# Optimization experiments

Measured on AMD Instinct MI355X. Metric: run time of the kernel, lower is better.

The kernel has to match this reference:

```python
import jax, jax.numpy as jnp
import numpy as np

D_MODEL = 1024
N_HEADS = 16
N_KV = 4
HEAD_DIM = D_MODEL // N_HEADS  # 64
EPS = 1e-5
THETA = 10000.0


def _rope_tables(S):
    half = HEAD_DIM // 2
    inv_freq = 1.0 / (THETA ** (jnp.arange(half, dtype=jnp.float32) / half))
    t = jnp.arange(S, dtype=jnp.float32)
    f = t[:, None] * inv_freq[None, :]  # [S, half]
    return jnp.cos(f), jnp.sin(f)


def _apply_rope(x, cos, sin):
    # x: [B, H, S, D]
    half = x.shape[-1] // 2
    x1, x2 = x[..., :half], x[..., half:]
    c = cos[None, None, :, :]
    s = sin[None, None, :, :]
    return jnp.concatenate([x1 * c - x2 * s, x1 * s + x2 * c], axis=-1)


def _rmsnorm(x, scale):
    rms = jnp.sqrt(jnp.mean(x * x, axis=-1, keepdims=True) + EPS)
    return x / rms * scale


def setup_inputs() -> dict:
    key = jax.random.key(0)
    ks = jax.random.split(key, 4)
    B, S = 2, 2048
    x = jax.random.normal(ks[0], (B, S, D_MODEL), dtype=jnp.float32)
    Wq = jax.random.normal(ks[1], (D_MODEL, D_MODEL), dtype=jnp.float32) * 0.02
    Wkv = jax.random.normal(ks[2], (D_MODEL, 2 * N_KV * HEAD_DIM), dtype=jnp.float32) * 0.02
    Wo = jax.random.normal(ks[3], (D_MODEL, D_MODEL), dtype=jnp.float32) * 0.02
    q_scale = jnp.ones((HEAD_DIM,), dtype=jnp.float32)
    k_scale = jnp.ones((HEAD_DIM,), dtype=jnp.float32)
    return {"x": x, "Wq": Wq, "Wkv": Wkv, "Wo": Wo,
            "q_scale": q_scale, "k_scale": k_scale}


def reference(x, Wq, Wkv, Wo, q_scale, k_scale):
    B, S, D = x.shape
    groups = N_HEADS // N_KV  # GQA group size

    # projections
    q = (x @ Wq).reshape(B, S, N_HEADS, HEAD_DIM).transpose(0, 2, 1, 3)  # [B,H,S,d]
    kv = x @ Wkv
    k, v = jnp.split(kv, 2, axis=-1)
    k = k.reshape(B, S, N_KV, HEAD_DIM).transpose(0, 2, 1, 3)  # [B,Hkv,S,d]
    v = v.reshape(B, S, N_KV, HEAD_DIM).transpose(0, 2, 1, 3)

    # per-head QK-RMSNorm (before RoPE, as in the torch module)
    q = _rmsnorm(q, q_scale)
    k = _rmsnorm(k, k_scale)

    # RoPE
    cos, sin = _rope_tables(S)
    q = _apply_rope(q, cos, sin)
    k = _apply_rope(k, cos, sin)

    # causal GQA attention (equivalent to SDPA with enable_gqa=True)
    qg = q.reshape(B, N_KV, groups, S, HEAD_DIM)
    scale = 1.0 / np.sqrt(HEAD_DIM).astype(np.float32)
    scores = jnp.einsum('bkgsd,bktd->bkgst', qg, k) * scale  # [B,Hkv,g,S,S]
    causal = jnp.tril(jnp.ones((S, S), dtype=bool))
    scores = jnp.where(causal[None, None, None], scores, -jnp.inf)
    attn = jax.nn.softmax(scores, axis=-1)
    out = jnp.einsum('bkgst,bktd->bkgsd', attn, v)
    out = out.reshape(B, N_HEADS, S, HEAD_DIM).transpose(0, 2, 1, 3).reshape(B, S, D)
    return out @ Wo
```

## Files before the change

kernel.cpp:

```cpp
#include <hip/hip_runtime.h>

#define S_LEN 2048
#define BATCH 2
#define DM    1024
#define NH    16
#define NKV   4
#define HD    64
#define MROWS (BATCH * S_LEN)
#define NQKV  1536

typedef __attribute__((ext_vector_type(8))) short bf16x8;
typedef __attribute__((ext_vector_type(4))) short s16x4;
typedef __attribute__((ext_vector_type(4))) float f32x4;

__device__ __forceinline__ unsigned short f2bf(float f) {
  unsigned int u = __float_as_uint(f);
  u += 0x7FFF + ((u >> 16) & 1);
  return (unsigned short)(u >> 16);
}

__device__ __forceinline__ void gload_lds16(const unsigned short* g, unsigned short* l) {
  __builtin_amdgcn_global_load_lds((const __attribute__((address_space(1))) void*)g,
                                   (__attribute__((address_space(3))) void*)l, 16, 0, 0);
}
__device__ __forceinline__ void gload_lds4(const unsigned short* g, unsigned short* l) {
  __builtin_amdgcn_global_load_lds((const __attribute__((address_space(1))) void*)g,
                                   (__attribute__((address_space(3))) void*)l, 4, 0, 0);
}

__global__ __launch_bounds__(256) void cvt_x_kernel(const float* __restrict__ x,
                                                    unsigned short* __restrict__ xb, int n) {
  int i = (blockIdx.x * 256 + threadIdx.x) * 4;
  if (i < n) {
    float4 v = *reinterpret_cast<const float4*>(x + i);
    xb[i + 0] = f2bf(v.x);
    xb[i + 1] = f2bf(v.y);
    xb[i + 2] = f2bf(v.z);
    xb[i + 3] = f2bf(v.w);
  }
}

__global__ __launch_bounds__(256) void transpose_all_kernel(const float* __restrict__ Wq,
                                                            const float* __restrict__ Wkv,
                                                            const float* __restrict__ Wo,
                                                            unsigned short* __restrict__ wt1,
                                                            unsigned short* __restrict__ wot) {
  __shared__ float tile[64][65];
  int bid = blockIdx.x;
  const float* in;
  unsigned short* out;
  int R, C, bx, by;
  if (bid < 256) { in = Wq; out = wt1; R = 1024; C = 1024; bx = bid & 15; by = bid >> 4; }
  else if (bid < 384) { int k = bid - 256; in = Wkv; out = wt1 + 1024 * 1024; R = 1024; C = 512; bx = k & 7; by = k >> 3; }
  else { int k = bid - 384; in = Wo; out = wot; R = 1024; C = 1024; bx = k & 15; by = k >> 4; }
  int r0 = by * 64, c0 = bx * 64;
  int t = threadIdx.x;
  int rl = t >> 2, cs = (t & 3) * 16;
#pragma unroll
  for (int k = 0; k < 4; ++k) {
    float4 v = *reinterpret_cast<const float4*>(in + (size_t)(r0 + rl) * C + c0 + cs + 4 * k);
    tile[rl][cs + 4 * k + 0] = v.x;
    tile[rl][cs + 4 * k + 1] = v.y;
    tile[rl][cs + 4 * k + 2] = v.z;
    tile[rl][cs + 4 * k + 3] = v.w;
  }
  __syncthreads();
  int cl = t >> 2, rs = (t & 3) * 16;
  bf16x8 v0, v1;
#pragma unroll
  for (int i = 0; i < 8; ++i) v0[i] = (short)f2bf(tile[rs + i][cl]);
#pragma unroll
  for (int i = 0; i < 8; ++i) v1[i] = (short)f2bf(tile[rs + 8 + i][cl]);
  unsigned short* dst = out + (size_t)(c0 + cl) * R + r0 + rs;
  *reinterpret_cast<bf16x8*>(dst) = v0;
  *reinterpret_cast<bf16x8*>(dst + 8) = v1;
}

__global__ __launch_bounds__(256) void gemm1_fused(const unsigned short* __restrict__ A,
                                                   const unsigned short* __restrict__ BT,
                                                   const float* __restrict__ q_scale,
                                                   const float* __restrict__ k_scale,
                                                   unsigned short* __restrict__ qb,
                                                   unsigned short* __restrict__ kbuf,
                                                   unsigned short* __restrict__ vrow,
                                                   int K) {
  __shared__ __align__(16) unsigned short As[128 * 64];
  __shared__ __align__(16) unsigned short Bs[64 * 64];
  int bx = blockIdx.x;
  int row0 = blockIdx.y * 128, col0 = bx * 64;
  int t = threadIdx.x;
  int w = t >> 6, lane = t & 63, quad = lane >> 4, l16 = lane & 15;
  int srow = lane >> 3;
  int scol = (lane & 7) * 8;

  f32x4 acc[2][4];
#pragma unroll
  for (int i = 0; i < 2; ++i)
#pragma unroll
    for (int j = 0; j < 4; ++j) acc[i][j] = (f32x4){0.f, 0.f, 0.f, 0.f};

  for (int k0 = 0; k0 < K; k0 += 64) {
#pragma unroll
    for (int j = 0; j < 4; ++j)
      gload_lds16(A + (size_t)(row0 + w * 32 + j * 8 + srow) * K + k0 + scol,
                  &As[(w * 32 + j * 8) * 64]);
#pragma unroll
    for (int j = 0; j < 2; ++j)
      gload_lds16(BT + (size_t)(col0 + w * 16 + j * 8 + srow) * K + k0 + scol,
                  &Bs[(w * 16 + j * 8) * 64]);
    __syncthreads();
#pragma unroll
    for (int ks = 0; ks < 2; ++ks) {
      bf16x8 af[2], bfr[4];
#pragma unroll
      for (int i = 0; i < 2; ++i)
        af[i] = *reinterpret_cast<const bf16x8*>(&As[(w * 32 + i * 16 + l16) * 64 + ks * 32 + quad * 8]);
#pragma unroll
      for (int j = 0; j < 4; ++j)
        bfr[j] = *reinterpret_cast<const bf16x8*>(&Bs[(j * 16 + l16) * 64 + ks * 32 + quad * 8]);
#pragma unroll
      for (int i = 0; i < 2; ++i)
#pragma unroll
        for (int j = 0; j < 4; ++j)
          acc[i][j] = __builtin_amdgcn_mfma_f32_16x16x32_bf16(af[i], bfr[j], acc[i][j], 0, 0, 0);
    }
    __syncthreads();
  }

  if (bx < 20) {
    const float* scale = (bx < 16) ? q_scale : k_scale;
    float post = (bx < 16) ? 1.0f : 0.125f * 1.44269504088896f;
    float sc0 = scale[l16], sc1 = scale[16 + l16], sc2 = scale[32 + l16], sc3 = scale[48 + l16];
    float invf0 = exp2f((float)l16 * (-13.2877123795495f / 32.0f));
    float invf1 = exp2f((float)(l16 + 16) * (-13.2877123795495f / 32.0f));
#pragma unroll
    for (int i = 0; i < 2; ++i)
#pragma unroll
      for (int rg = 0; rg < 4; ++rg) {
        int row = row0 + w * 32 + i * 16 + quad * 4 + rg;
        int b = row >> 11, s = row & 2047;
        float v0 = acc[i][0][rg], v1 = acc[i][1][rg], v2 = acc[i][2][rg], v3 = acc[i][3][rg];
        float ss = v0 * v0 + v1 * v1 + v2 * v2 + v3 * v3;
        ss += __shfl_xor(ss, 1, 64);
        ss += __shfl_xor(ss, 2, 64);
        ss += __shfl_xor(ss, 4, 64);
        ss += __shfl_xor(ss, 8, 64);
        float inv_rms = 1.0f / sqrtf(ss * (1.0f / 64.0f) + 1e-5f);
        float n0 = v0 * inv_rms * sc0, n1 = v1 * inv_rms * sc1;
        float n2 = v2 * inv_rms * sc2, n3 = v3 * inv_rms * sc3;
        float f0 = (float)s * invf0, f1 = (float)s * invf1;
        float c0 = cosf(f0), s0 = sinf(f0), c1 = cosf(f1), s1 = sinf(f1);
        float o0 = (n0 * c0 - n2 * s0) * post;
        float o1 = (n1 * c1 - n3 * s1) * post;
        float o2 = (n0 * s0 + n2 * c0) * post;
        float o3 = (n1 * s1 + n3 * c1) * post;
        unsigned short* dst = (bx < 16)
            ? qb + ((size_t)(b * NH + bx) * S_LEN + s) * HD
            : kbuf + ((size_t)(b * NKV + (bx - 16)) * S_LEN + s) * HD;
        dst[l16] = f2bf(o0);
        dst[16 + l16] = f2bf(o1);
        dst[32 + l16] = f2bf(o2);
        dst[48 + l16] = f2bf(o3);
      }
  } else {
    int kvh = bx - 20;
#pragma unroll
    for (int i = 0; i < 2; ++i)
#pragma unroll
      for (int rg = 0; rg < 4; ++rg) {
        int row = row0 + w * 32 + i * 16 + quad * 4 + rg;
        unsigned short* dst = vrow + (size_t)row * 256 + kvh * 64;
        dst[l16] = f2bf(acc[i][0][rg]);
        dst[16 + l16] = f2bf(acc[i][1][rg]);
        dst[32 + l16] = f2bf(acc[i][2][rg]);
        dst[48 + l16] = f2bf(acc[i][3][rg]);
      }
  }
}

__global__ __launch_bounds__(256) void v_transpose_bf16(const unsigned short* __restrict__ vrow,
                                                        unsigned short* __restrict__ vt) {
  __shared__ unsigned short tile[64][72];
  int bkv = blockIdx.x >> 5;
  int b = bkv >> 2, kvh = bkv & 3;
  int s0 = (blockIdx.x & 31) * 64;
  int t = threadIdx.x;
  int sl = t >> 2, part = (t & 3) * 16;
  const unsigned short* src = vrow + (size_t)(b * S_LEN + s0 + sl) * 256 + kvh * 64 + part;
  *reinterpret_cast<bf16x8*>(&tile[sl][part]) = *reinterpret_cast<const bf16x8*>(src);
  *reinterpret_cast<bf16x8*>(&tile[sl][part + 8]) = *reinterpret_cast<const bf16x8*>(src + 8);
  __syncthreads();
  int d = t >> 2, sc = (t & 3) * 16;
  bf16x8 a0, a1;
#pragma unroll
  for (int i = 0; i < 8; ++i) a0[i] = (short)tile[sc + i][d];
#pragma unroll
  for (int i = 0; i < 8; ++i) a1[i] = (short)tile[sc + 8 + i][d];
  unsigned short* dst = vt + ((size_t)bkv * 64 + d) * S_LEN + s0 + sc;
  *reinterpret_cast<bf16x8*>(dst) = a0;
  *reinterpret_cast<bf16x8*>(dst + 8) = a1;
}

#define CH 136
#define TILE_SH (32 * CH)
__global__ __launch_bounds__(256, 3) void attn_kernel(const unsigned short* __restrict__ qb,
                                                      const unsigned short* __restrict__ kbuf,
                                                      const unsigned short* __restrict__ vt,
                                                      unsigned short* __restrict__ Opart,
                                                      float* __restrict__ lpart) {
  __shared__ __align__(16) unsigned short Ks[2][TILE_SH];
  __shared__ __align__(16) unsigned short Vs[2][TILE_SH];
  __shared__ __align__(16) unsigned short PT[4][2][16][72];
  const size_t OZ = (size_t)BATCH * NH * S_LEN * HD;
  const size_t LZ = (size_t)BATCH * NH * S_LEN;
  int t32 = 63 - (int)(blockIdx.x >> 4);
  int sub = blockIdx.x & 15;
  int z = sub & 1;
  int bkv = sub >> 1;
  int b = bkv >> 2, kvh = bkv & 3;
  int w = threadIdx.x >> 6;
  int h = kvh * 4 + w;
  int lane = threadIdx.x & 63;
  int quad = lane >> 4, l16 = lane & 15;
  int qa = t32 * 32 + l16;
  const unsigned short* Q = qb + (size_t)(b * NH + h) * S_LEN * HD;
  const unsigned short* Kh = kbuf + (size_t)(b * NKV + kvh) * S_LEN * HD;
  const unsigned short* Vh = vt + (size_t)(b * NKV + kvh) * HD * S_LEN;

  bf16x8 bqa0 = *reinterpret_cast<const bf16x8*>(Q + (size_t)qa * HD + quad * 8);
  bf16x8 bqa1 = *reinterpret_cast<const bf16x8*>(Q + (size_t)qa * HD + 32 + quad * 8);
  bf16x8 bqb0 = *reinterpret_cast<const bf16x8*>(Q + (size_t)(qa + 16) * HD + quad * 8);
  bf16x8 bqb1 = *reinterpret_cast<const bf16x8*>(Q + (size_t)(qa + 16) * HD + 32 + quad * 8);

  bf16x8 ones;
#pragma unroll
  for (int i = 0; i < 8; ++i) ones[i] = (short)0x3F80;

  f32x4 ot[2][4];
#pragma unroll
  for (int gq = 0; gq < 2; ++gq)
#pragma unroll
    for (int i = 0; i < 4; ++i) ot[gq][i] = (f32x4){0.f, 0.f, 0.f, 0.f};
  f32x4 ol[2] = {(f32x4){0.f, 0.f, 0.f, 0.f}, (f32x4){0.f, 0.f, 0.f, 0.f}};

  int n = (t32 >> 1) + 1;

  auto stage = [&](int kbase, int dbuf) {
    const unsigned short* kg = Kh + (size_t)(kbase + w * 16) * HD + lane * 2;
    const unsigned short* vg = Vh + (size_t)(w * 16 + (lane >> 5)) * S_LEN + kbase + (lane & 31) * 2;
    unsigned short* kl = &Ks[dbuf][(w * 8) * CH];
    unsigned short* vl = &Vs[dbuf][(w * 8) * CH];
#pragma unroll
    for (int c = 0; c < 8; ++c) {
      gload_lds4(kg + (size_t)(2 * c) * HD, kl + c * CH);
      gload_lds4(vg + (size_t)(2 * c) * S_LEN, vl + c * CH);
    }
  };

  if (z < n) {
    stage(z << 6, 0);
    __syncthreads();

    for (int kb = z; kb < n; kb += 2) {
      int dbuf = (kb >> 1) & 1;
      bool diag = (kb == n - 1);
      if (kb + 2 < n) stage((kb + 2) << 6, dbuf ^ 1);
      int kbase = kb << 6;
      const unsigned short* Kd = Ks[dbuf];
      const unsigned short* Vd = Vs[dbuf];

      f32x4 sa[4], sb[4];
#pragma unroll
      for (int km = 0; km < 4; ++km) {
        int ch = km * 8 + (l16 >> 1);
        int base = ch * CH + (l16 & 1) * 64;
        bf16x8 k0 = *reinterpret_cast<const bf16x8*>(&Kd[base + quad * 8]);
        bf16x8 k1 = *reinterpret_cast<const bf16x8*>(&Kd[base + 32 + quad * 8]);
        f32x4 s = {0.f, 0.f, 0.f, 0.f};
        s = __builtin_amdgcn_mfma_f32_16x16x32_bf16(k0, bqa0, s, 0, 0, 0);
        s = __builtin_amdgcn_mfma_f32_16x16x32_bf16(k1, bqa1, s, 0, 0, 0);
        sa[km] = s;
        f32x4 s2 = {0.f, 0.f, 0.f, 0.f};
        s2 = __builtin_amdgcn_mfma_f32_16x16x32_bf16(k0, bqb0, s2, 0, 0, 0);
        s2 = __builtin_amdgcn_mfma_f32_16x16x32_bf16(k1, bqb1, s2, 0, 0, 0);
        sb[km] = s2;
      }
      if (diag) {
#pragma unroll
        for (int km = 0; km < 4; ++km)
#pragma unroll
          for (int rg = 0; rg < 4; ++rg) {
            int key = kbase + km * 16 + quad * 4 + rg;
            if (key > qa) sa[km][rg] = -1e30f;
            if (key > qa + 16) sb[km][rg] = -1e30f;
          }
      }
#pragma unroll
      for (int km = 0; km < 4; ++km) {
        float a0 = exp2f(sa[km][0]), a1 = exp2f(sa[km][1]);
        float a2 = exp2f(sa[km][2]), a3 = exp2f(sa[km][3]);
        uint2 pw;
        pw.x = __builtin_amdgcn_perm(__float_as_uint(a1), __float_as_uint(a0), 0x07060302);
        pw.y = __builtin_amdgcn_perm(__float_as_uint(a3), __float_as_uint(a2), 0x07060302);
        *reinterpret_cast<uint2*>(&PT[w][0][l16][km * 16 + quad * 4]) = pw;
        float b0 = exp2f(sb[km][0]), b1 = exp2f(sb[km][1]);
        float b2 = exp2f(sb[km][2]), b3 = exp2f(sb[km][3]);
        uint2 qw;
        qw.x = __builtin_amdgcn_perm(__float_as_uint(b1), __float_as_uint(b0), 0x07060302);
        qw.y = __builtin_amdgcn_perm(__float_as_uint(b3), __float_as_uint(b2), 0x07060302);
        *reinterpret_cast<uint2*>(&PT[w][1][l16][km * 16 + quad * 4]) = qw;
      }
      bf16x8 pa0 = *reinterpret_cast<const bf16x8*>(&PT[w][0][l16][quad * 8]);
      bf16x8 pa1 = *reinterpret_cast<const bf16x8*>(&PT[w][0][l16][32 + quad * 8]);
      bf16x8 pb0 = *reinterpret_cast<const bf16x8*>(&PT[w][1][l16][quad * 8]);
      bf16x8 pb1 = *reinterpret_cast<const bf16x8*>(&PT[w][1][l16][32 + quad * 8]);
      ol[0] = __builtin_amdgcn_mfma_f32_16x16x32_bf16(ones, pa0, ol[0], 0, 0, 0);
      ol[0] = __builtin_amdgcn_mfma_f32_16x16x32_bf16(ones, pa1, ol[0], 0, 0, 0);
      ol[1] = __builtin_amdgcn_mfma_f32_16x16x32_bf16(ones, pb0, ol[1], 0, 0, 0);
      ol[1] = __builtin_amdgcn_mfma_f32_16x16x32_bf16(ones, pb1, ol[1], 0, 0, 0);
#pragma unroll
      for (int dm = 0; dm < 4; ++dm) {
        int ch = dm * 8 + (l16 >> 1);
        int base = ch * CH + (l16 & 1) * 64;
        bf16x8 v0 = *reinterpret_cast<const bf16x8*>(&Vd[base + quad * 8]);
        bf16x8 v1 = *reinterpret_cast<const bf16x8*>(&Vd[base + 32 + quad * 8]);
        ot[0][dm] = __builtin_amdgcn_mfma_f32_16x16x32_bf16(v0, pa0, ot[0][dm], 0, 0, 0);
        ot[0][dm] = __builtin_amdgcn_mfma_f32_16x16x32_bf16(v1, pa1, ot[0][dm], 0, 0, 0);
        ot[1][dm] = __builtin_amdgcn_mfma_f32_16x16x32_bf16(v0, pb0, ot[1][dm], 0, 0, 0);
        ot[1][dm] = __builtin_amdgcn_mfma_f32_16x16x32_bf16(v1, pb1, ot[1][dm], 0, 0, 0);
      }
      __syncthreads();
    }
  }

  unsigned short* Oz = Opart + (size_t)z * OZ;
  float* lz = lpart + (size_t)z * LZ;
#pragma unroll
  for (int gq = 0; gq < 2; ++gq) {
    size_t base = ((size_t)(b * NH + h) * S_LEN + qa + gq * 16) * HD;
#pragma unroll
    for (int dm = 0; dm < 4; ++dm) {
      s16x4 pv;
#pragma unroll
      for (int rg = 0; rg < 4; ++rg) pv[rg] = (short)f2bf(ot[gq][dm][rg]);
      *reinterpret_cast<s16x4*>(Oz + base + dm * 16 + quad * 4) = pv;
    }
  }
  if (quad == 0) {
    size_t lb = (size_t)(b * NH + h) * S_LEN + t32 * 32 + l16;
    lz[lb] = ol[0][0];
    lz[lb + 16] = ol[1][0];
  }
}

__global__ __launch_bounds__(256) void attn_combine_kernel(const unsigned short* __restrict__ Opart,
                                                           const float* __restrict__ lpart,
                                                           unsigned short* __restrict__ ctx) {
  const size_t OZ = (size_t)BATCH * NH * S_LEN * HD;
  const size_t LZ = (size_t)BATCH * NH * S_LEN;
  int i8 = blockIdx.x * 256 + threadIdx.x;
  size_t i = (size_t)i8 * 8;
  int row = i8 >> 3;
  bf16x8 a = *reinterpret_cast<const bf16x8*>(Opart + i);
  bf16x8 c = *reinterpret_cast<const bf16x8*>(Opart + OZ + i);
  float inv = 1.0f / (lpart[row] + lpart[LZ + row]);
  int q = row & 2047;
  int bh = row >> 11;
  int b = bh >> 4, h = bh & 15;
  int d0 = (i8 & 7) * 8;
  bf16x8 o;
#pragma unroll
  for (int k = 0; k < 8; ++k) {
    float fa = __uint_as_float(((unsigned int)(unsigned short)a[k]) << 16);
    float fc = __uint_as_float(((unsigned int)(unsigned short)c[k]) << 16);
    o[k] = (short)f2bf((fa + fc) * inv);
  }
  *reinterpret_cast<bf16x8*>(ctx + ((size_t)(b * S_LEN + q)) * DM + h * HD + d0) = o;
}

__global__ __launch_bounds__(256) void gemm_bt_n64(const unsigned short* __restrict__ A,
                                                   const unsigned short* __restrict__ BT,
                                                   float* __restrict__ C,
                                                   int M, int N, int K) {
  __shared__ __align__(16) unsigned short As[128 * 64];
  __shared__ __align__(16) unsigned short Bs[64 * 64];
  int row0 = blockIdx.y * 128, col0 = blockIdx.x * 64;
  int t = threadIdx.x;
  int w = t >> 6, lane = t & 63, quad = lane >> 4, l16 = lane & 15;
  int srow = lane >> 3;
  int scol = (lane & 7) * 8;

  f32x4 acc[2][4];
#pragma unroll
  for (int i = 0; i < 2; ++i)
#pragma unroll
    for (int j = 0; j < 4; ++j) acc[i][j] = (f32x4){0.f, 0.f, 0.f, 0.f};

  for (int k0 = 0; k0 < K; k0 += 64) {
#pragma unroll
    for (int j = 0; j < 4; ++j)
      gload_lds16(A + (size_t)(row0 + w * 32 + j * 8 + srow) * K + k0 + scol,
                  &As[(w * 32 + j * 8) * 64]);
#pragma unroll
    for (int j = 0; j < 2; ++j)
      gload_lds16(BT + (size_t)(col0 + w * 16 + j * 8 + srow) * K + k0 + scol,
                  &Bs[(w * 16 + j * 8) * 64]);
    __syncthreads();
#pragma unroll
    for (int ks = 0; ks < 2; ++ks) {
      bf16x8 af[2], bfr[4];
#pragma unroll
      for (int i = 0; i < 2; ++i)
        af[i] = *reinterpret_cast<const bf16x8*>(&As[(w * 32 + i * 16 + l16) * 64 + ks * 32 + quad * 8]);
#pragma unroll
      for (int j = 0; j < 4; ++j)
        bfr[j] = *reinterpret_cast<const bf16x8*>(&Bs[(j * 16 + l16) * 64 + ks * 32 + quad * 8]);
#pragma unroll
      for (int i = 0; i < 2; ++i)
#pragma unroll
        for (int j = 0; j < 4; ++j)
          acc[i][j] = __builtin_amdgcn_mfma_f32_16x16x32_bf16(af[i], bfr[j], acc[i][j], 0, 0, 0);
    }
    __syncthreads();
  }
#pragma unroll
  for (int i = 0; i < 2; ++i)
#pragma unroll
    for (int j = 0; j < 4; ++j) {
      int row = row0 + w * 32 + i * 16 + quad * 4;
      float* Cptr = C + (size_t)row * N + col0 + j * 16 + l16;
#pragma unroll
      for (int rg = 0; rg < 4; ++rg) Cptr[(size_t)rg * N] = acc[i][j][rg];
    }
}

extern "C" void kernel_launch(void* const* d_in, const int* in_sizes, int n_in,
                              void* d_out, int out_size, void* d_ws, size_t ws_size,
                              hipStream_t stream) {
  const float* x = (const float*)d_in[0];
  const float* Wq = (const float*)d_in[1];
  const float* Wkv = (const float*)d_in[2];
  const float* Wo = (const float*)d_in[3];
  const float* q_scale = (const float*)d_in[4];
  const float* k_scale = (const float*)d_in[5];
  float* out = (float*)d_out;

  char* ws = (char*)d_ws;
  size_t off = 0;
  auto alloc = [&](size_t bytes) {
    void* p = ws + off;
    off += (bytes + 255) & ~(size_t)255;
    return p;
  };
  unsigned short* xb = (unsigned short*)alloc((size_t)MROWS * DM * 2);
  unsigned short* wt1 = (unsigned short*)alloc((size_t)NQKV * DM * 2);
  unsigned short* wot = (unsigned short*)alloc((size_t)DM * DM * 2);
  unsigned short* qb = (unsigned short*)alloc((size_t)BATCH * NH * S_LEN * HD * 2);
  unsigned short* kbuf = (unsigned short*)alloc((size_t)BATCH * NKV * S_LEN * HD * 2);
  unsigned short* vrow = (unsigned short*)alloc((size_t)MROWS * NKV * HD * 2);
  unsigned short* vt = (unsigned short*)alloc((size_t)BATCH * NKV * HD * S_LEN * 2);
  unsigned short* ctx = (unsigned short*)alloc((size_t)MROWS * DM * 2);
  unsigned short* Opart = (unsigned short*)alloc(2 * (size_t)BATCH * NH * S_LEN * HD * 2);
  float* lpart = (float*)alloc(2 * (size_t)BATCH * NH * S_LEN * 4);

  cvt_x_kernel<<<(MROWS * DM) / 1024, 256, 0, stream>>>(x, xb, MROWS * DM);
  transpose_all_kernel<<<640, 256, 0, stream>>>(Wq, Wkv, Wo, wt1, wot);

  gemm1_fused<<<dim3(NQKV / 64, MROWS / 128), 256, 0, stream>>>(xb, wt1, q_scale, k_scale,
                                                                qb, kbuf, vrow, DM);
  v_transpose_bf16<<<256, 256, 0, stream>>>(vrow, vt);

  attn_kernel<<<1024, 256, 0, stream>>>(qb, kbuf, vt, Opart, lpart);
  attn_combine_kernel<<<(BATCH * NH * S_LEN * HD / 8) / 256, 256, 0, stream>>>(Opart, lpart, ctx);

  gemm_bt_n64<<<dim3(DM / 64, MROWS / 128), 256, 0, stream>>>(ctx, wot, out, MROWS, DM, DM);
}
```

Measured before the change: 175.7 us.

## Load K/V fragments directly from global memory instead of LDS staging

Removes the double-buffered LDS staging of K and V tiles via global_load_lds and the per-iteration block barrier. Each wave now loads its K and V MFMA operand fragments straight from global memory into registers. This frees LDS, which could raise occupancy, and removes the sync cost. In exchange, each of the four waves loads the same K/V data separately, which relies on L1/L2 hits, and there is no prefetch overlap, so load latency is exposed.

```diff
diff --git a/kernel.cpp b/kernel.cpp
--- a/kernel.cpp
+++ b/kernel.cpp
@@ -22,10 +22,6 @@
 __device__ __forceinline__ void gload_lds16(const unsigned short* g, unsigned short* l) {
   __builtin_amdgcn_global_load_lds((const __attribute__((address_space(1))) void*)g,
                                    (__attribute__((address_space(3))) void*)l, 16, 0, 0);
-}
-__device__ __forceinline__ void gload_lds4(const unsigned short* g, unsigned short* l) {
-  __builtin_amdgcn_global_load_lds((const __attribute__((address_space(1))) void*)g,
-                                   (__attribute__((address_space(3))) void*)l, 4, 0, 0);
 }
 
 __global__ __launch_bounds__(256) void cvt_x_kernel(const float* __restrict__ x,
@@ -201,15 +197,11 @@
   *reinterpret_cast<bf16x8*>(dst + 8) = a1;
 }
 
-#define CH 136
-#define TILE_SH (32 * CH)
 __global__ __launch_bounds__(256, 3) void attn_kernel(const unsigned short* __restrict__ qb,
                                                       const unsigned short* __restrict__ kbuf,
                                                       const unsigned short* __restrict__ vt,
                                                       unsigned short* __restrict__ Opart,
                                                       float* __restrict__ lpart) {
-  __shared__ __align__(16) unsigned short Ks[2][TILE_SH];
-  __shared__ __align__(16) unsigned short Vs[2][TILE_SH];
   __shared__ __align__(16) unsigned short PT[4][2][16][72];
   const size_t OZ = (size_t)BATCH * NH * S_LEN * HD;
   const size_t LZ = (size_t)BATCH * NH * S_LEN;
@@ -245,46 +237,40 @@
 
   int n = (t32 >> 1) + 1;
 
-  auto stage = [&](int kbase, int dbuf) {
-    const unsigned short* kg = Kh + (size_t)(kbase + w * 16) * HD + lane * 2;
-    const unsigned short* vg = Vh + (size_t)(w * 16 + (lane >> 5)) * S_LEN + kbase + (lane & 31) * 2;
-    unsigned short* kl = &Ks[dbuf][(w * 8) * CH];
-    unsigned short* vl = &Vs[dbuf][(w * 8) * CH];
-#pragma unroll
-    for (int c = 0; c < 8; ++c) {
-      gload_lds4(kg + (size_t)(2 * c) * HD, kl + c * CH);
-      gload_lds4(vg + (size_t)(2 * c) * S_LEN, vl + c * CH);
-    }
-  };
-
   if (z < n) {
-    stage(z << 6, 0);
-    __syncthreads();
-
     for (int kb = z; kb < n; kb += 2) {
-      int dbuf = (kb >> 1) & 1;
       bool diag = (kb == n - 1);
-      if (kb + 2 < n) stage((kb + 2) << 6, dbuf ^ 1);
       int kbase = kb << 6;
-      const unsigned short* Kd = Ks[dbuf];
-      const unsigned short* Vd = Vs[dbuf];
+
+      bf16x8 kf[4][2];
+#pragma unroll
+      for (int km = 0; km < 4; ++km) {
+        const unsigned short* kp = Kh + (size_t)(kbase + km * 16 + l16) * HD + quad * 8;
+        kf[km][0] = *reinterpret_cast<const bf16x8*>(kp);
+        kf[km][1] = *reinterpret_cast<const bf16x8*>(kp + 32);
+      }
 
       f32x4 sa[4], sb[4];
 #pragma unroll
       for (int km = 0; km < 4; ++km) {
-        int ch = km * 8 + (l16 >> 1);
-        int base = ch * CH + (l16 & 1) * 64;
-        bf16x8 k0 = *reinterpret_cast<const bf16x8*>(&Kd[base + quad * 8]);
-        bf16x8 k1 = *reinterpret_cast<const bf16x8*>(&Kd[base + 32 + quad * 8]);
         f32x4 s = {0.f, 0.f, 0.f, 0.f};
-        s = __builtin_amdgcn_mfma_f32_16x16x32_bf16(k0, bqa0, s, 0, 0, 0);
-        s = __builtin_amdgcn_mfma_f32_16x16x32_bf16(k1, bqa1, s, 0, 0, 0);
+        s = __builtin_amdgcn_mfma_f32_16x16x32_bf16(kf[km][0], bqa0, s, 0, 0, 0);
+        s = __builtin_amdgcn_mfma_f32_16x16x32_bf16(kf[km][1], bqa1, s, 0, 0, 0);
         sa[km] = s;
         f32x4 s2 = {0.f, 0.f, 0.f, 0.f};
-        s2 = __builtin_amdgcn_mfma_f32_16x16x32_bf16(k0, bqb0, s2, 0, 0, 0);
-        s2 = __builtin_amdgcn_mfma_f32_16x16x32_bf16(k1, bqb1, s2, 0, 0, 0);
+        s2 = __builtin_amdgcn_mfma_f32_16x16x32_bf16(kf[km][0], bqb0, s2, 0, 0, 0);
+        s2 = __builtin_amdgcn_mfma_f32_16x16x32_bf16(kf[km][1], bqb1, s2, 0, 0, 0);
         sb[km] = s2;
       }
+
+      bf16x8 vf[4][2];
+#pragma unroll
+      for (int dm = 0; dm < 4; ++dm) {
+        const unsigned short* vp = Vh + (size_t)(dm * 16 + l16) * S_LEN + kbase + quad * 8;
+        vf[dm][0] = *reinterpret_cast<const bf16x8*>(vp);
+        vf[dm][1] = *reinterpret_cast<const bf16x8*>(vp + 32);
+      }
+
       if (diag) {
 #pragma unroll
         for (int km = 0; km < 4; ++km)
@@ -320,16 +306,11 @@
       ol[1] = __builtin_amdgcn_mfma_f32_16x16x32_bf16(ones, pb1, ol[1], 0, 0, 0);
 #pragma unroll
       for (int dm = 0; dm < 4; ++dm) {
-        int ch = dm * 8 + (l16 >> 1);
-        int base = ch * CH + (l16 & 1) * 64;
-        bf16x8 v0 = *reinterpret_cast<const bf16x8*>(&Vd[base + quad * 8]);
-        bf16x8 v1 = *reinterpret_cast<const bf16x8*>(&Vd[base + 32 + quad * 8]);
-        ot[0][dm] = __builtin_amdgcn_mfma_f32_16x16x32_bf16(v0, pa0, ot[0][dm], 0, 0, 0);
-        ot[0][dm] = __builtin_amdgcn_mfma_f32_16x16x32_bf16(v1, pa1, ot[0][dm], 0, 0, 0);
-        ot[1][dm] = __builtin_amdgcn_mfma_f32_16x16x32_bf16(v0, pb0, ot[1][dm], 0, 0, 0);
-        ot[1][dm] = __builtin_amdgcn_mfma_f32_16x16x32_bf16(v1, pb1, ot[1][dm], 0, 0, 0);
-      }
-      __syncthreads();
+        ot[0][dm] = __builtin_amdgcn_mfma_f32_16x16x32_bf16(vf[dm][0], pa0, ot[0][dm], 0, 0, 0);
+        ot[0][dm] = __builtin_amdgcn_mfma_f32_16x16x32_bf16(vf[dm][1], pa1, ot[0][dm], 0, 0, 0);
+        ot[1][dm] = __builtin_amdgcn_mfma_f32_16x16x32_bf16(vf[dm][0], pb0, ot[1][dm], 0, 0, 0);
+        ot[1][dm] = __builtin_amdgcn_mfma_f32_16x16x32_bf16(vf[dm][1], pb1, ot[1][dm], 0, 0, 0);
+      }
     }
   }
 
```

Result: slower. 210.6 us (+19.9%).

## Permute K row mapping so P stays in registers; merge prep kernels

Applied to the files above, without the earlier changes.

The attention kernel now remaps which key rows each lane loads from K in LDS. The QK^T MFMA output then lands in the layout the PV MFMA needs as its B operand, so the bf16 probabilities are packed straight into registers. This removes the per-tile LDS round trip through the PT buffer and frees that shared memory. Separately, the x conversion and weight transpose kernels are merged into one launch to save one kernel launch, at the cost of the LDS tile being allocated for the elementwise blocks too.

```diff
diff --git a/kernel.cpp b/kernel.cpp
--- a/kernel.cpp
+++ b/kernel.cpp
@@ -12,6 +12,7 @@
 typedef __attribute__((ext_vector_type(8))) short bf16x8;
 typedef __attribute__((ext_vector_type(4))) short s16x4;
 typedef __attribute__((ext_vector_type(4))) float f32x4;
+typedef __attribute__((ext_vector_type(4))) int i32x4;
 
 __device__ __forceinline__ unsigned short f2bf(float f) {
   unsigned int u = __float_as_uint(f);
@@ -28,33 +29,34 @@
                                    (__attribute__((address_space(3))) void*)l, 4, 0, 0);
 }
 
-__global__ __launch_bounds__(256) void cvt_x_kernel(const float* __restrict__ x,
-                                                    unsigned short* __restrict__ xb, int n) {
-  int i = (blockIdx.x * 256 + threadIdx.x) * 4;
-  if (i < n) {
+__global__ __launch_bounds__(256) void prep_kernel(const float* __restrict__ x,
+                                                   unsigned short* __restrict__ xb,
+                                                   const float* __restrict__ Wq,
+                                                   const float* __restrict__ Wkv,
+                                                   const float* __restrict__ Wo,
+                                                   unsigned short* __restrict__ wt1,
+                                                   unsigned short* __restrict__ wot) {
+  __shared__ float tile[64][65];
+  int bid = blockIdx.x;
+  int t = threadIdx.x;
+  if (bid < 4096) {
+    int i = (bid * 256 + t) * 4;
     float4 v = *reinterpret_cast<const float4*>(x + i);
     xb[i + 0] = f2bf(v.x);
     xb[i + 1] = f2bf(v.y);
     xb[i + 2] = f2bf(v.z);
     xb[i + 3] = f2bf(v.w);
-  }
-}
-
-__global__ __launch_bounds__(256) void transpose_all_kernel(const float* __restrict__ Wq,
-                                                            const float* __restrict__ Wkv,
-                                                            const float* __restrict__ Wo,
-                                                            unsigned short* __restrict__ wt1,
-                                                            unsigned short* __restrict__ wot) {
-  __shared__ float tile[64][65];
-  int bid = blockIdx.x;
+    return;
+  }
+  bid -= 4096;
   const float* in;
   unsigned short* out;
-  int R, C, bx, by;
-  if (bid < 256) { in = Wq; out = wt1; R = 1024; C = 1024; bx = bid & 15; by = bid >> 4; }
-  else if (bid < 384) { int k = bid - 256; in = Wkv; out = wt1 + 1024 * 1024; R = 1024; C = 512; bx = k & 7; by = k >> 3; }
-  else { int k = bid - 384; in = Wo; out = wot; R = 1024; C = 1024; bx = k & 15; by = k >> 4; }
+  int C, bx, by;
+  if (bid < 256) { in = Wq; out = wt1; C = 1024; bx = bid & 15; by = bid >> 4; }
+  else if (bid < 384) { int k = bid - 256; in = Wkv; out = wt1 + 1024 * 1024; C = 512; bx = k & 7; by = k >> 3; }
+  else { int k = bid - 384; in = Wo; out = wot; C = 1024; bx = k & 15; by = k >> 4; }
+  const int R = 1024;
   int r0 = by * 64, c0 = bx * 64;
-  int t = threadIdx.x;
   int rl = t >> 2, cs = (t & 3) * 16;
 #pragma unroll
   for (int k = 0; k < 4; ++k) {
@@ -210,7 +212,6 @@
                                                       float* __restrict__ lpart) {
   __shared__ __align__(16) unsigned short Ks[2][TILE_SH];
   __shared__ __align__(16) unsigned short Vs[2][TILE_SH];
-  __shared__ __align__(16) unsigned short PT[4][2][16][72];
   const size_t OZ = (size_t)BATCH * NH * S_LEN * HD;
   const size_t LZ = (size_t)BATCH * NH * S_LEN;
   int t32 = 63 - (int)(blockIdx.x >> 4);
@@ -272,8 +273,8 @@
       f32x4 sa[4], sb[4];
 #pragma unroll
       for (int km = 0; km < 4; ++km) {
-        int ch = km * 8 + (l16 >> 1);
-        int base = ch * CH + (l16 & 1) * 64;
+        int kk = 32 * (km >> 1) + 4 * (km & 1) + 8 * (l16 >> 2) + (l16 & 3);
+        int base = (kk >> 1) * CH + (kk & 1) * 64;
         bf16x8 k0 = *reinterpret_cast<const bf16x8*>(&Kd[base + quad * 8]);
         bf16x8 k1 = *reinterpret_cast<const bf16x8*>(&Kd[base + 32 + quad * 8]);
         f32x4 s = {0.f, 0.f, 0.f, 0.f};
@@ -290,30 +291,31 @@
         for (int km = 0; km < 4; ++km)
 #pragma unroll
           for (int rg = 0; rg < 4; ++rg) {
-            int key = kbase + km * 16 + quad * 4 + rg;
+            int key = kbase + 32 * (km >> 1) + 8 * quad + 4 * (km & 1) + rg;
             if (key > qa) sa[km][rg] = -1e30f;
             if (key > qa + 16) sb[km][rg] = -1e30f;
           }
       }
+      unsigned int pk[4][2], qk[4][2];
 #pragma unroll
       for (int km = 0; km < 4; ++km) {
         float a0 = exp2f(sa[km][0]), a1 = exp2f(sa[km][1]);
         float a2 = exp2f(sa[km][2]), a3 = exp2f(sa[km][3]);
-        uint2 pw;
-        pw.x = __builtin_amdgcn_perm(__float_as_uint(a1), __float_as_uint(a0), 0x07060302);
-        pw.y = __builtin_amdgcn_perm(__float_as_uint(a3), __float_as_uint(a2), 0x07060302);
-        *reinterpret_cast<uint2*>(&PT[w][0][l16][km * 16 + quad * 4]) = pw;
+        pk[km][0] = __builtin_amdgcn_perm(__float_as_uint(a1), __float_as_uint(a0), 0x07060302);
+        pk[km][1] = __builtin_amdgcn_perm(__float_as_uint(a3), __float_as_uint(a2), 0x07060302);
         float b0 = exp2f(sb[km][0]), b1 = exp2f(sb[km][1]);
         float b2 = exp2f(sb[km][2]), b3 = exp2f(sb[km][3]);
-        uint2 qw;
-        qw.x = __builtin_amdgcn_perm(__float_as_uint(b1), __float_as_uint(b0), 0x07060302);
-        qw.y = __builtin_amdgcn_perm(__float_as_uint(b3), __float_as_uint(b2), 0x07060302);
-        *reinterpret_cast<uint2*>(&PT[w][1][l16][km * 16 + quad * 4]) = qw;
-      }
-      bf16x8 pa0 = *reinterpret_cast<const bf16x8*>(&PT[w][0][l16][quad * 8]);
-      bf16x8 pa1 = *reinterpret_cast<const bf16x8*>(&PT[w][0][l16][32 + quad * 8]);
-      bf16x8 pb0 = *reinterpret_cast<const bf16x8*>(&PT[w][1][l16][quad * 8]);
-      bf16x8 pb1 = *reinterpret_cast<const bf16x8*>(&PT[w][1][l16][32 + quad * 8]);
+        qk[km][0] = __builtin_amdgcn_perm(__float_as_uint(b1), __float_as_uint(b0), 0x07060302);
+        qk[km][1] = __builtin_amdgcn_perm(__float_as_uint(b3), __float_as_uint(b2), 0x07060302);
+      }
+      i32x4 wa0 = {(int)pk[0][0], (int)pk[0][1], (int)pk[1][0], (int)pk[1][1]};
+      i32x4 wa1 = {(int)pk[2][0], (int)pk[2][1], (int)pk[3][0], (int)pk[3][1]};
+      i32x4 wb0 = {(int)qk[0][0], (int)qk[0][1], (int)qk[1][0], (int)qk[1][1]};
+      i32x4 wb1 = {(int)qk[2][0], (int)qk[2][1], (int)qk[3][0], (int)qk[3][1]};
+      bf16x8 pa0 = *reinterpret_cast<bf16x8*>(&wa0);
+      bf16x8 pa1 = *reinterpret_cast<bf16x8*>(&wa1);
+      bf16x8 pb0 = *reinterpret_cast<bf16x8*>(&wb0);
+      bf16x8 pb1 = *reinterpret_cast<bf16x8*>(&wb1);
       ol[0] = __builtin_amdgcn_mfma_f32_16x16x32_bf16(ones, pa0, ol[0], 0, 0, 0);
       ol[0] = __builtin_amdgcn_mfma_f32_16x16x32_bf16(ones, pa1, ol[0], 0, 0, 0);
       ol[1] = __builtin_amdgcn_mfma_f32_16x16x32_bf16(ones, pb0, ol[1], 0, 0, 0);
@@ -463,8 +465,7 @@
   unsigned short* Opart = (unsigned short*)alloc(2 * (size_t)BATCH * NH * S_LEN * HD * 2);
   float* lpart = (float*)alloc(2 * (size_t)BATCH * NH * S_LEN * 4);
 
-  cvt_x_kernel<<<(MROWS * DM) / 1024, 256, 0, stream>>>(x, xb, MROWS * DM);
-  transpose_all_kernel<<<640, 256, 0, stream>>>(Wq, Wkv, Wo, wt1, wot);
+  prep_kernel<<<4736, 256, 0, stream>>>(x, xb, Wq, Wkv, Wo, wt1, wot);
 
   gemm1_fused<<<dim3(NQKV / 64, MROWS / 128), 256, 0, stream>>>(xb, wt1, q_scale, k_scale,
                                                                 qb, kbuf, vrow, DM);
```

Measured after the change: 174.6 us. Within noise of the previous version (-0.7%).
